# Kernel optimization log

Hardware: AMD Instinct MI355X
Metric: run time of the kernel (lower is better)

The kernel has to match this reference:

```python
import jax, jax.numpy as jnp
import numpy as np

N_NODES = 100000
N_EDGES = 3200000
NODE_DIM = 128
MRI_DIM, COG_DIM, CLIN_DIM, GEN_DIM = 256, 64, 32, 512
N_GRAPHS = 256
N_CLASSES = 3
HID = 16


def setup_inputs() -> dict:
    key = jax.random.key(0)
    ks = jax.random.split(key, 20)
    inp = {
        "x": jax.random.normal(ks[0], (N_NODES, NODE_DIM), jnp.float32),
        "edge_index": jax.random.randint(ks[1], (2, N_EDGES), 0, N_NODES, jnp.int64),
        "batch": jnp.sort(jax.random.randint(ks[2], (N_NODES,), 0, N_GRAPHS, jnp.int64)),
        "mri": jax.random.normal(ks[3], (N_GRAPHS, MRI_DIM), jnp.float32),
        "cog": jax.random.normal(ks[4], (N_GRAPHS, COG_DIM), jnp.float32),
        "clin": jax.random.normal(ks[5], (N_GRAPHS, CLIN_DIM), jnp.float32),
        "genetic": jax.random.normal(ks[6], (N_GRAPHS, GEN_DIM), jnp.float32),
        # GCNConv weight/bias
        "gcn_W": jax.random.normal(ks[7], (NODE_DIM, HID), jnp.float32) / np.sqrt(NODE_DIM),
        "gcn_b": jnp.zeros((HID,), jnp.float32),
        # modality FCs (each -> 4)
        "mri_W": jax.random.normal(ks[8], (MRI_DIM, 4), jnp.float32) / np.sqrt(MRI_DIM),
        "mri_b": jnp.zeros((4,), jnp.float32),
        "cog_W": jax.random.normal(ks[9], (COG_DIM, 4), jnp.float32) / np.sqrt(COG_DIM),
        "cog_b": jnp.zeros((4,), jnp.float32),
        "clin_W": jax.random.normal(ks[10], (CLIN_DIM, 4), jnp.float32) / np.sqrt(CLIN_DIM),
        "clin_b": jnp.zeros((4,), jnp.float32),
        "gen_W": jax.random.normal(ks[11], (GEN_DIM, 4), jnp.float32) / np.sqrt(GEN_DIM),
        "gen_b": jnp.zeros((4,), jnp.float32),
        # classifier: Linear(32,16) -> ReLU -> Dropout(eval: identity) -> Linear(16,3)
        "cls_W1": jax.random.normal(ks[12], (32, HID), jnp.float32) / np.sqrt(32.0),
        "cls_b1": jnp.zeros((HID,), jnp.float32),
        "cls_W2": jax.random.normal(ks[13], (HID, N_CLASSES), jnp.float32) / np.sqrt(HID),
        "cls_b2": jnp.zeros((N_CLASSES,), jnp.float32),
    }
    return inp


def gcn_conv(x, edge_index, W, b):
    # PyG GCNConv: add self-loops, symmetric normalization, scatter-add.
    n = x.shape[0]
    xw = x @ W  # [N, HID]
    loop = jnp.arange(n, dtype=edge_index.dtype)
    src = jnp.concatenate([edge_index[0], loop])
    dst = jnp.concatenate([edge_index[1], loop])
    deg = jax.ops.segment_sum(jnp.ones_like(dst, dtype=xw.dtype), dst, num_segments=n)
    dinv = jnp.where(deg > 0, jax.lax.rsqrt(deg), 0.0)
    norm = dinv[src] * dinv[dst]  # [E+N]
    msg = xw[src] * norm[:, None]  # gather + scale
    out = jax.ops.segment_sum(msg, dst, num_segments=n)  # scatter-add
    return out + b


def global_mean_pool(feat, batch, num_graphs):
    s = jax.ops.segment_sum(feat, batch, num_segments=num_graphs)
    cnt = jax.ops.segment_sum(jnp.ones((feat.shape[0],), feat.dtype), batch, num_segments=num_graphs)
    return s / jnp.maximum(cnt, 1.0)[:, None]


def reference(x, edge_index, batch, mri, cog, clin, genetic,
              gcn_W, gcn_b, mri_W, mri_b, cog_W, cog_b, clin_W, clin_b,
              gen_W, gen_b, cls_W1, cls_b1, cls_W2, cls_b2):
    g = jax.nn.relu(gcn_conv(x, edge_index, gcn_W, gcn_b))  # [N, 16]
    g_emb = global_mean_pool(g, batch, N_GRAPHS)            # [B, 16]
    m = jax.nn.relu(mri @ mri_W + mri_b)
    c = jax.nn.relu(cog @ cog_W + cog_b)
    cl = jax.nn.relu(clin @ clin_W + clin_b)
    ge = jax.nn.relu(genetic @ gen_W + gen_b)
    mm = jnp.concatenate([m, c, cl, ge], axis=1)            # [B, 16]
    comb = jnp.concatenate([g_emb, mm], axis=1)             # [B, 32]
    h = jax.nn.relu(comb @ cls_W1 + cls_b1)                 # dropout is identity in eval
    logits = h @ cls_W2 + cls_b2
    return jax.nn.log_softmax(logits, axis=1)
```

## Files before the change

kernel.cpp:

```cpp
#include <hip/hip_runtime.h>
#include <hip/hip_bf16.h>
#include <math.h>

#define N_NODES   100000
#define N_EDGES   3200000
#define NODE_DIM  128
#define HID       16
#define N_GRAPHS  256

#define BSHIFT    6
#define NPB       64
#define NBUCK     ((N_NODES + NPB - 1) >> BSHIFT)
#define NBLK      256
#define TOT       (NBUCK * NBLK)
#define ACC64S    9

#define FIX16  4096.0f
#define IFIX16 (1.0f/4096.0f)
#define FIXP   131072.0f
#define IFIXP  (1.0f/131072.0f)

__device__ __forceinline__ short f2bf(float f) {
    unsigned u = __float_as_uint(f);
    unsigned r = (u + 0x7FFF + ((u >> 16) & 1)) >> 16;
    return (short)r;
}
__device__ __forceinline__ int fx(float v, float s) { return __float2int_rn(v * s); }

__device__ __forceinline__ unsigned long long packA(int w) {
    return ((unsigned long long)(unsigned)(w >> 16) << 32)
         | (unsigned)((w & 0xFFFF) ^ 0x8000);
}

typedef __attribute__((ext_vector_type(8))) short bf16x8;
typedef __attribute__((ext_vector_type(4))) float f32x4;
typedef __attribute__((ext_vector_type(4))) int   i32x4;

__global__ __launch_bounds__(1024) void bucket_count(
    const int* __restrict__ dst, int* __restrict__ Mc, int E, int chunk)
{
    __shared__ int cnt[NBUCK];
    const int t = threadIdx.x, b = blockIdx.x;
    for (int k = t; k < NBUCK; k += 1024) cnt[k] = 0;
    __syncthreads();
    int e0 = b * chunk, e1 = min(E, e0 + chunk);
    if (e1 > e0) {
        const int4* d4 = (const int4*)dst;
        for (int i = (e0 >> 2) + t; i < (e1 >> 2); i += 1024) {
            int4 d = d4[i];
            atomicAdd(&cnt[d.x >> BSHIFT], 1);
            atomicAdd(&cnt[d.y >> BSHIFT], 1);
            atomicAdd(&cnt[d.z >> BSHIFT], 1);
            atomicAdd(&cnt[d.w >> BSHIFT], 1);
        }
    }
    __syncthreads();
    for (int k = t; k < NBUCK; k += 1024) Mc[b * NBUCK + k] = cnt[k];
}

__global__ __launch_bounds__(256) void transpose_M(
    const int* __restrict__ A, int* __restrict__ At)
{
    __shared__ int tile[64][65];
    const int kt = blockIdx.x * 64, bt = blockIdx.y * 64;
    const int t = threadIdx.x, tr = t >> 6, tc = t & 63;
    for (int i = tr; i < 64; i += 4) {
        int b = bt + i, k = kt + tc;
        tile[i][tc] = (k < NBUCK) ? A[b * NBUCK + k] : 0;
    }
    __syncthreads();
    for (int i = tr; i < 64; i += 4) {
        int k = kt + i, b = bt + tc;
        if (k < NBUCK) At[k * NBLK + b] = tile[tc][i];
    }
}

__global__ __launch_bounds__(256) void scan_blocksum(
    const int* __restrict__ M, int* __restrict__ bsum, int n)
{
    __shared__ int red[256];
    int t = threadIdx.x;
    int base = blockIdx.x * 2048 + t * 8;
    int s = 0;
    #pragma unroll
    for (int k = 0; k < 8; ++k) { int i = base + k; if (i < n) s += M[i]; }
    red[t] = s; __syncthreads();
    for (int o = 128; o > 0; o >>= 1) {
        if (t < o) red[t] += red[t + o];
        __syncthreads();
    }
    if (t == 0) bsum[blockIdx.x] = red[0];
}

__global__ __launch_bounds__(256) void scan_write2(
    int* __restrict__ M, const int* __restrict__ bsum, int n, int nb)
{
    __shared__ int tmp[256];
    __shared__ int tsum[256];
    int t = threadIdx.x;
    tmp[t] = (t < nb) ? bsum[t] : 0;
    __syncthreads();
    for (int o = 1; o < 256; o <<= 1) {
        int a = (t >= o) ? tmp[t - o] : 0;
        __syncthreads();
        tmp[t] += a;
        __syncthreads();
    }
    const int pre0 = (blockIdx.x > 0) ? tmp[blockIdx.x - 1] : 0;

    int base = blockIdx.x * 2048 + t * 8;
    int v[8]; int s = 0;
    #pragma unroll
    for (int k = 0; k < 8; ++k) { int i = base + k; v[k] = (i < n) ? M[i] : 0; s += v[k]; }
    tsum[t] = s; __syncthreads();
    int mine = s;
    for (int o = 1; o < 256; o <<= 1) {
        int a = (t >= o) ? tsum[t - o] : 0;
        __syncthreads();
        tsum[t] += a;
        __syncthreads();
    }
    int pre = pre0 + tsum[t] - mine;
    #pragma unroll
    for (int k = 0; k < 8; ++k) {
        int i = base + k;
        if (i < n) { M[i] = pre; pre += v[k]; }
    }
}

__global__ __launch_bounds__(1024) void bucket_scatter(
    const int* __restrict__ src, const int* __restrict__ dst,
    const int* __restrict__ offT, int* __restrict__ ebuf, int E, int chunk)
{
    __shared__ int cur[NBUCK];
    const int t = threadIdx.x;
    const int b = (blockIdx.x & 7) * (NBLK >> 3) + (blockIdx.x >> 3);
    for (int k = t; k < NBUCK; k += 1024) cur[k] = offT[k * NBLK + b];
    __syncthreads();
    int e0 = b * chunk, e1 = min(E, e0 + chunk);
    if (e1 <= e0) return;
    const i32x4* d4 = (const i32x4*)dst;
    const i32x4* s4 = (const i32x4*)src;
    for (int i = (e0 >> 2) + t; i < (e1 >> 2); i += 1024) {
        i32x4 d = __builtin_nontemporal_load(&d4[i]);
        i32x4 s = __builtin_nontemporal_load(&s4[i]);
        int p;
        p = atomicAdd(&cur[d[0] >> BSHIFT], 1); ebuf[p] = s[0] | ((d[0] & (NPB-1)) << 17);
        p = atomicAdd(&cur[d[1] >> BSHIFT], 1); ebuf[p] = s[1] | ((d[1] & (NPB-1)) << 17);
        p = atomicAdd(&cur[d[2] >> BSHIFT], 1); ebuf[p] = s[2] | ((d[2] & (NPB-1)) << 17);
        p = atomicAdd(&cur[d[3] >> BSHIFT], 1); ebuf[p] = s[3] | ((d[3] & (NPB-1)) << 17);
    }
}

__global__ __launch_bounds__(256) void degxw_kernel(
    const int* __restrict__ offT, const int* __restrict__ ebuf,
    const float* __restrict__ x, const float* __restrict__ W,
    float* __restrict__ dinv, int* __restrict__ degA,
    short* __restrict__ xws16, int N, int E)
{
    __shared__ int hist4[4][72];
    __shared__ float dloc[NPB];
    const int k = blockIdx.x, t = threadIdx.x;
    const int base = k << BSHIFT;
    const int wave = t >> 6;

    {
        int* hp = &hist4[0][0];
        for (int i = t; i < 4 * 72; i += 256) hp[i] = 0;
    }
    __syncthreads();
    {
        int start = offT[k * NBLK];
        int end = (k == NBUCK - 1) ? E : offT[(k + 1) * NBLK];
        for (int j = start + t; j < end; j += 256)
            atomicAdd(&hist4[wave][ebuf[j] >> 17], 1);
    }
    __syncthreads();
    if (t < NPB) {
        int dd = hist4[0][t] + hist4[1][t] + hist4[2][t] + hist4[3][t];
        float dv = rsqrtf((float)(dd + 1));
        dloc[t] = dv;
        if (base + t < N) { dinv[base + t] = dv; degA[base + t] = dd; }
    }
    __syncthreads();

    const int lane = t & 63;
    const int q = lane >> 4, n = lane & 15;
    const int tile_base = base + (t >> 6) * 16;
    if (tile_base >= N) return;

    bf16x8 bfrag[4];
    #pragma unroll
    for (int i = 0; i < 4; ++i)
        #pragma unroll
        for (int j = 0; j < 8; ++j)
            bfrag[i][j] = f2bf(W[(i * 32 + q * 8 + j) * HID + n]);

    const float4* x4 = (const float4*)x;
    const int node = tile_base + n;
    f32x4 d = {0.f, 0.f, 0.f, 0.f};
    #pragma unroll
    for (int i = 0; i < 4; ++i) {
        float4 u0 = make_float4(0.f, 0.f, 0.f, 0.f), u1 = u0;
        if (node < N) {
            u0 = x4[(size_t)node * 32 + i * 8 + q * 2];
            u1 = x4[(size_t)node * 32 + i * 8 + q * 2 + 1];
        }
        bf16x8 a;
        a[0] = f2bf(u0.x); a[1] = f2bf(u0.y); a[2] = f2bf(u0.z); a[3] = f2bf(u0.w);
        a[4] = f2bf(u1.x); a[5] = f2bf(u1.y); a[6] = f2bf(u1.z); a[7] = f2bf(u1.w);
        d = __builtin_amdgcn_mfma_f32_16x16x32_bf16(a, bfrag[i], d, 0, 0, 0);
    }
    #pragma unroll
    for (int r = 0; r < 4; ++r) {
        int nd = tile_base + q * 4 + r;
        if (nd < N) {
            float val = d[r] * dloc[nd - base];
            val = fminf(7.995f, fmaxf(-7.995f, val));
            xws16[(size_t)nd * HID + n] = (short)__float2int_rn(val * FIX16);
        }
    }
}

__global__ __launch_bounds__(256, 8) void gather_pool(
    const int* __restrict__ offT, const int* __restrict__ ebuf,
    const float* __restrict__ dinv, const int* __restrict__ degA,
    const short* __restrict__ xws16, const float* __restrict__ gcn_b,
    const int* __restrict__ batch, int* __restrict__ pool,
    int* __restrict__ cnt, int N, int E)
{
    __shared__ unsigned long long acc64[NPB * ACC64S];
    __shared__ int lpool[16 * HID];
    __shared__ int lcnt[16];
    const int k = blockIdx.x, t = threadIdx.x;
    const int base = k << BSHIFT;

    for (int i = t; i < NPB * ACC64S; i += 256) acc64[i] = 0ull;
    lpool[t] = 0;
    if (t < 16) lcnt[t] = 0;

    const int start = offT[k * NBLK];
    const int end = (k == NBUCK - 1) ? E : offT[(k + 1) * NBLK];
    const int Ek = end - start;
    __syncthreads();

    const int sub = t >> 1, h = t & 1;
    const int4* xw4 = (const int4*)xws16;
    const int* eb = ebuf + start;

    int e = sub;
    for (; e + 7 * 128 < Ek; e += 1024) {
        int w[8]; int4 vv[8];
        #pragma unroll
        for (int u = 0; u < 8; ++u) w[u] = eb[e + u * 128];
        #pragma unroll
        for (int u = 0; u < 8; ++u) vv[u] = xw4[(size_t)(w[u] & 0x1FFFF) * 2 + h];
        #pragma unroll
        for (int u = 0; u < 8; ++u) {
            unsigned long long* p = &acc64[(w[u] >> 17) * ACC64S + h * 4];
            atomicAdd(p + 0, packA(vv[u].x));
            atomicAdd(p + 1, packA(vv[u].y));
            atomicAdd(p + 2, packA(vv[u].z));
            atomicAdd(p + 3, packA(vv[u].w));
        }
    }
    for (; e < Ek; e += 128) {
        int w = eb[e];
        int4 vv = xw4[(size_t)(w & 0x1FFFF) * 2 + h];
        unsigned long long* p = &acc64[(w >> 17) * ACC64S + h * 4];
        atomicAdd(p + 0, packA(vv.x));
        atomicAdd(p + 1, packA(vv.y));
        atomicAdd(p + 2, packA(vv.z));
        atomicAdd(p + 3, packA(vv.w));
    }
    __syncthreads();

    int nN = min(NPB, N - base);
    int gmin = batch[base], gmax = batch[base + nN - 1];
    int range = gmax - gmin + 1;
    bool useL = (range <= 16);
    const int sub16 = t >> 4, lane16 = t & 15;
    float bb = gcn_b[lane16];

    for (int i = sub16; i < nN; i += 16) {
        int n = base + i;
        unsigned long long word = acc64[i * ACC64S + (lane16 >> 1)];
        int s = (lane16 & 1)
              ? (int)(unsigned)(word >> 32)
              : (int)(unsigned)(word & 0xFFFFFFFFull) - degA[n] * 32768;
        int tot = s + (int)xws16[(size_t)n * HID + lane16];
        float a = (float)tot * IFIX16;
        float r = fmaxf(fmaf(dinv[n], a, bb), 0.f);
        int g = batch[n];
        int ri = fx(r, FIXP);
        if (useL) {
            atomicAdd(&lpool[(g - gmin) * HID + lane16], ri);
            if (lane16 == 0) atomicAdd(&lcnt[g - gmin], 1);
        } else {
            atomicAdd(&pool[g * HID + lane16], ri);
            if (lane16 == 0) atomicAdd(&cnt[g], 1);
        }
    }
    __syncthreads();

    if (useL) {
        for (int i = t; i < range * HID; i += 256) {
            int vv = lpool[i];
            if (vv != 0) atomicAdd(&pool[gmin * HID + i], vv);
        }
        for (int i = t; i < range; i += 256) {
            int c = lcnt[i];
            if (c != 0) atomicAdd(&cnt[gmin + i], c);
        }
    }
}

__global__ __launch_bounds__(64) void head_kernel(
    const int* __restrict__ pool, const int* __restrict__ cnt,
    const float* __restrict__ mri,  const float* __restrict__ cog,
    const float* __restrict__ clin, const float* __restrict__ gen,
    const float* __restrict__ mriW, const float* __restrict__ mrib,
    const float* __restrict__ cogW, const float* __restrict__ cogb,
    const float* __restrict__ clinW, const float* __restrict__ clinb,
    const float* __restrict__ genW, const float* __restrict__ genb,
    const float* __restrict__ W1, const float* __restrict__ b1,
    const float* __restrict__ W2, const float* __restrict__ b2,
    float* __restrict__ out)
{
    const int g = blockIdx.x;
    const int lane = threadIdx.x;
    __shared__ float comb[32];
    __shared__ float h[HID];

    if (lane < HID) {
        float c = fmaxf((float)cnt[g], 1.f);
        comb[lane] = ((float)pool[g * HID + lane] * IFIXP) / c;
    }

    struct Mod { const float* in; const float* W; const float* b; int K; int off; };
    Mod mods[4] = {
        { mri  + (size_t)g * 256, mriW,  mrib,  256, 16 },
        { cog  + (size_t)g * 64,  cogW,  cogb,  64,  20 },
        { clin + (size_t)g * 32,  clinW, clinb, 32,  24 },
        { gen  + (size_t)g * 512, genW,  genb,  512, 28 },
    };
    for (int m = 0; m < 4; ++m) {
        float p0 = 0.f, p1 = 0.f, p2 = 0.f, p3 = 0.f;
        const float* in = mods[m].in;
        const float* Wm = mods[m].W;
        for (int kk = lane; kk < mods[m].K; kk += 64) {
            float xv = in[kk];
            p0 += xv * Wm[kk * 4 + 0];
            p1 += xv * Wm[kk * 4 + 1];
            p2 += xv * Wm[kk * 4 + 2];
            p3 += xv * Wm[kk * 4 + 3];
        }
        #pragma unroll
        for (int o = 32; o > 0; o >>= 1) {
            p0 += __shfl_down(p0, o);
            p1 += __shfl_down(p1, o);
            p2 += __shfl_down(p2, o);
            p3 += __shfl_down(p3, o);
        }
        if (lane == 0) {
            const float* bm = mods[m].b;
            int o = mods[m].off;
            comb[o + 0] = fmaxf(p0 + bm[0], 0.f);
            comb[o + 1] = fmaxf(p1 + bm[1], 0.f);
            comb[o + 2] = fmaxf(p2 + bm[2], 0.f);
            comb[o + 3] = fmaxf(p3 + bm[3], 0.f);
        }
    }
    __syncthreads();

    if (lane < HID) {
        float a = b1[lane];
        #pragma unroll
        for (int kk = 0; kk < 32; ++kk) a += comb[kk] * W1[kk * HID + lane];
        h[lane] = fmaxf(a, 0.f);
    }
    __syncthreads();

    if (lane == 0) {
        float l0 = b2[0], l1 = b2[1], l2 = b2[2];
        #pragma unroll
        for (int kk = 0; kk < HID; ++kk) {
            float hv = h[kk];
            l0 += hv * W2[kk * 3 + 0];
            l1 += hv * W2[kk * 3 + 1];
            l2 += hv * W2[kk * 3 + 2];
        }
        float mx = fmaxf(l0, fmaxf(l1, l2));
        float lse = mx + logf(expf(l0 - mx) + expf(l1 - mx) + expf(l2 - mx));
        out[g * 3 + 0] = l0 - lse;
        out[g * 3 + 1] = l1 - lse;
        out[g * 3 + 2] = l2 - lse;
    }
}

extern "C" void kernel_launch(void* const* d_in, const int* in_sizes, int n_in,
                              void* d_out, int out_size, void* d_ws, size_t ws_size,
                              hipStream_t stream)
{
    const float* x     = (const float*)d_in[0];
    const int*   eidx  = (const int*)d_in[1];
    const int*   batch = (const int*)d_in[2];
    const float* mri   = (const float*)d_in[3];
    const float* cog   = (const float*)d_in[4];
    const float* clin  = (const float*)d_in[5];
    const float* gen   = (const float*)d_in[6];
    const float* gcn_W = (const float*)d_in[7];
    const float* gcn_b = (const float*)d_in[8];
    const float* mriW  = (const float*)d_in[9];
    const float* mrib  = (const float*)d_in[10];
    const float* cogW  = (const float*)d_in[11];
    const float* cogb  = (const float*)d_in[12];
    const float* clinW = (const float*)d_in[13];
    const float* clinb = (const float*)d_in[14];
    const float* genW  = (const float*)d_in[15];
    const float* genb  = (const float*)d_in[16];
    const float* W1    = (const float*)d_in[17];
    const float* b1    = (const float*)d_in[18];
    const float* W2    = (const float*)d_in[19];
    const float* b2    = (const float*)d_in[20];
    float* out = (float*)d_out;

    const int N = in_sizes[0] / NODE_DIM;
    const int E = in_sizes[1] / 2;
    const int* src = eidx;
    const int* dst = eidx + E;

    float* ws    = (float*)d_ws;
    short* xws16 = (short*)ws;
    float* dinv  = ws + 800000;
    int*   pool  = (int*)(ws + 900000);
    int*   cnt   = (int*)(ws + 904096);
    int*   Mc    = (int*)(ws + 905000);
    int*   offT  = (int*)(ws + 1306000);
    int*   bsum  = (int*)(ws + 2108000);
    int*   ebuf  = (int*)(ws + 2109000);
    int*   degA  = (int*)(ws + 5309000);

    const int chunkE = (E + NBLK - 1) / NBLK;
    const int scanNB = (TOT + 2047) / 2048;
    const dim3 tgrid((NBUCK + 63) / 64, NBLK / 64);

    hipMemsetAsync(pool, 0, (N_GRAPHS * HID + N_GRAPHS) * sizeof(int), stream);

    bucket_count<<<NBLK, 1024, 0, stream>>>(dst, Mc, E, chunkE);
    transpose_M<<<tgrid, 256, 0, stream>>>(Mc, offT);
    scan_blocksum<<<scanNB, 256, 0, stream>>>(offT, bsum, TOT);
    scan_write2<<<scanNB, 256, 0, stream>>>(offT, bsum, TOT, scanNB);
    bucket_scatter<<<NBLK, 1024, 0, stream>>>(src, dst, offT, ebuf, E, chunkE);
    degxw_kernel<<<NBUCK, 256, 0, stream>>>(offT, ebuf, x, gcn_W, dinv, degA, xws16, N, E);
    gather_pool<<<NBUCK, 256, 0, stream>>>(offT, ebuf, dinv, degA, xws16,
                                           gcn_b, batch, pool, cnt, N, E);
    head_kernel<<<N_GRAPHS, 64, 0, stream>>>(
        pool, cnt, mri, cog, clin, gen,
        mriW, mrib, cogW, cogb, clinW, clinb, genW, genb,
        W1, b1, W2, b2, out);
}
```

Before: 224.2 us.

## Compute x@W in extra blocks of the bucket-count kernel, rescale by dinv later

The dense x@W MFMA projection is moved out of the degree kernel into extra blocks appended to the edge-bucket counting launch. It therefore runs alongside the atomic-bound counting and the 51MB read of x overlaps other work. The degree kernel becomes a histogram plus an in-place rescale of the fixed-point xw values by dinv. The cost is an extra read-modify-write of the 16-bit xw buffer and a second rounding, with the clamp now applied before scaling, which slightly changes precision.

```diff
diff --git a/kernel.cpp b/kernel.cpp
--- a/kernel.cpp
+++ b/kernel.cpp
@@ -36,26 +36,70 @@
 typedef __attribute__((ext_vector_type(4))) float f32x4;
 typedef __attribute__((ext_vector_type(4))) int   i32x4;
 
-__global__ __launch_bounds__(1024) void bucket_count(
-    const int* __restrict__ dst, int* __restrict__ Mc, int E, int chunk)
+__global__ __launch_bounds__(1024) void count_xw(
+    const int* __restrict__ dst, int* __restrict__ Mc,
+    const float* __restrict__ x, const float* __restrict__ W,
+    short* __restrict__ xws16, int N, int E, int chunk)
 {
     __shared__ int cnt[NBUCK];
-    const int t = threadIdx.x, b = blockIdx.x;
-    for (int k = t; k < NBUCK; k += 1024) cnt[k] = 0;
-    __syncthreads();
-    int e0 = b * chunk, e1 = min(E, e0 + chunk);
-    if (e1 > e0) {
-        const int4* d4 = (const int4*)dst;
-        for (int i = (e0 >> 2) + t; i < (e1 >> 2); i += 1024) {
-            int4 d = d4[i];
-            atomicAdd(&cnt[d.x >> BSHIFT], 1);
-            atomicAdd(&cnt[d.y >> BSHIFT], 1);
-            atomicAdd(&cnt[d.z >> BSHIFT], 1);
-            atomicAdd(&cnt[d.w >> BSHIFT], 1);
-        }
-    }
-    __syncthreads();
-    for (int k = t; k < NBUCK; k += 1024) Mc[b * NBUCK + k] = cnt[k];
+    const int t = threadIdx.x;
+
+    if (blockIdx.x < NBLK) {
+        const int b = blockIdx.x;
+        for (int k = t; k < NBUCK; k += 1024) cnt[k] = 0;
+        __syncthreads();
+        int e0 = b * chunk, e1 = min(E, e0 + chunk);
+        if (e1 > e0) {
+            const int4* d4 = (const int4*)dst;
+            for (int i = (e0 >> 2) + t; i < (e1 >> 2); i += 1024) {
+                int4 d = d4[i];
+                atomicAdd(&cnt[d.x >> BSHIFT], 1);
+                atomicAdd(&cnt[d.y >> BSHIFT], 1);
+                atomicAdd(&cnt[d.z >> BSHIFT], 1);
+                atomicAdd(&cnt[d.w >> BSHIFT], 1);
+            }
+        }
+        __syncthreads();
+        for (int k = t; k < NBUCK; k += 1024) Mc[b * NBUCK + k] = cnt[k];
+        return;
+    }
+
+    const int kb = blockIdx.x - NBLK;
+    const int lane = t & 63;
+    const int q = lane >> 4, n = lane & 15;
+    const int tile_base = kb * 256 + (t >> 6) * 16;
+    if (tile_base >= N) return;
+
+    bf16x8 bfrag[4];
+    #pragma unroll
+    for (int i = 0; i < 4; ++i)
+        #pragma unroll
+        for (int j = 0; j < 8; ++j)
+            bfrag[i][j] = f2bf(W[(i * 32 + q * 8 + j) * HID + n]);
+
+    const float4* x4 = (const float4*)x;
+    const int node = tile_base + n;
+    f32x4 d = {0.f, 0.f, 0.f, 0.f};
+    #pragma unroll
+    for (int i = 0; i < 4; ++i) {
+        float4 u0 = make_float4(0.f, 0.f, 0.f, 0.f), u1 = u0;
+        if (node < N) {
+            u0 = x4[(size_t)node * 32 + i * 8 + q * 2];
+            u1 = x4[(size_t)node * 32 + i * 8 + q * 2 + 1];
+        }
+        bf16x8 a;
+        a[0] = f2bf(u0.x); a[1] = f2bf(u0.y); a[2] = f2bf(u0.z); a[3] = f2bf(u0.w);
+        a[4] = f2bf(u1.x); a[5] = f2bf(u1.y); a[6] = f2bf(u1.z); a[7] = f2bf(u1.w);
+        d = __builtin_amdgcn_mfma_f32_16x16x32_bf16(a, bfrag[i], d, 0, 0, 0);
+    }
+    #pragma unroll
+    for (int r = 0; r < 4; ++r) {
+        int nd = tile_base + q * 4 + r;
+        if (nd < N) {
+            float val = fminf(7.995f, fmaxf(-7.995f, d[r]));
+            xws16[(size_t)nd * HID + n] = (short)__float2int_rn(val * FIX16);
+        }
+    }
 }
 
 __global__ __launch_bounds__(256) void transpose_M(
@@ -152,9 +196,8 @@
     }
 }
 
-__global__ __launch_bounds__(256) void degxw_kernel(
+__global__ __launch_bounds__(256) void hist_scale(
     const int* __restrict__ offT, const int* __restrict__ ebuf,
-    const float* __restrict__ x, const float* __restrict__ W,
     float* __restrict__ dinv, int* __restrict__ degA,
     short* __restrict__ xws16, int N, int E)
 {
@@ -184,41 +227,16 @@
     }
     __syncthreads();
 
-    const int lane = t & 63;
-    const int q = lane >> 4, n = lane & 15;
-    const int tile_base = base + (t >> 6) * 16;
-    if (tile_base >= N) return;
-
-    bf16x8 bfrag[4];
-    #pragma unroll
-    for (int i = 0; i < 4; ++i)
-        #pragma unroll
-        for (int j = 0; j < 8; ++j)
-            bfrag[i][j] = f2bf(W[(i * 32 + q * 8 + j) * HID + n]);
-
-    const float4* x4 = (const float4*)x;
-    const int node = tile_base + n;
-    f32x4 d = {0.f, 0.f, 0.f, 0.f};
-    #pragma unroll
-    for (int i = 0; i < 4; ++i) {
-        float4 u0 = make_float4(0.f, 0.f, 0.f, 0.f), u1 = u0;
-        if (node < N) {
-            u0 = x4[(size_t)node * 32 + i * 8 + q * 2];
-            u1 = x4[(size_t)node * 32 + i * 8 + q * 2 + 1];
-        }
-        bf16x8 a;
-        a[0] = f2bf(u0.x); a[1] = f2bf(u0.y); a[2] = f2bf(u0.z); a[3] = f2bf(u0.w);
-        a[4] = f2bf(u1.x); a[5] = f2bf(u1.y); a[6] = f2bf(u1.z); a[7] = f2bf(u1.w);
-        d = __builtin_amdgcn_mfma_f32_16x16x32_bf16(a, bfrag[i], d, 0, 0, 0);
-    }
-    #pragma unroll
-    for (int r = 0; r < 4; ++r) {
-        int nd = tile_base + q * 4 + r;
-        if (nd < N) {
-            float val = d[r] * dloc[nd - base];
-            val = fminf(7.995f, fmaxf(-7.995f, val));
-            xws16[(size_t)nd * HID + n] = (short)__float2int_rn(val * FIX16);
-        }
+    int nN = min(NPB, N - base);
+    int* xp = (int*)(xws16 + (size_t)base * HID);
+    int nI = nN * 8;
+    for (int i = t; i < nI; i += 256) {
+        int v = xp[i];
+        float dv = dloc[i >> 3];
+        int lo = (v << 16) >> 16, hi = v >> 16;
+        int nlo = __float2int_rn((float)lo * dv);
+        int nhi = __float2int_rn((float)hi * dv);
+        xp[i] = (nlo & 0xFFFF) | (nhi << 16);
     }
 }
 
@@ -443,16 +461,17 @@
 
     const int chunkE = (E + NBLK - 1) / NBLK;
     const int scanNB = (TOT + 2047) / 2048;
+    const int nxw = (N + 255) / 256;
     const dim3 tgrid((NBUCK + 63) / 64, NBLK / 64);
 
     hipMemsetAsync(pool, 0, (N_GRAPHS * HID + N_GRAPHS) * sizeof(int), stream);
 
-    bucket_count<<<NBLK, 1024, 0, stream>>>(dst, Mc, E, chunkE);
+    count_xw<<<NBLK + nxw, 1024, 0, stream>>>(dst, Mc, x, gcn_W, xws16, N, E, chunkE);
     transpose_M<<<tgrid, 256, 0, stream>>>(Mc, offT);
     scan_blocksum<<<scanNB, 256, 0, stream>>>(offT, bsum, TOT);
     scan_write2<<<scanNB, 256, 0, stream>>>(offT, bsum, TOT, scanNB);
     bucket_scatter<<<NBLK, 1024, 0, stream>>>(src, dst, offT, ebuf, E, chunkE);
-    degxw_kernel<<<NBUCK, 256, 0, stream>>>(offT, ebuf, x, gcn_W, dinv, degA, xws16, N, E);
+    hist_scale<<<NBUCK, 256, 0, stream>>>(offT, ebuf, dinv, degA, xws16, N, E);
     gather_pool<<<NBUCK, 256, 0, stream>>>(offT, ebuf, dinv, degA, xws16,
                                            gcn_b, batch, pool, cnt, N, E);
     head_kernel<<<N_GRAPHS, 64, 0, stream>>>(
```

New measurement: 228.0 us. About the same (+1.7%).
